# Performance work log

Measured on AMD Instinct MI355X. Metric: run time of the kernel, lower is better.

## Reference

```python
import jax, jax.numpy as jnp
import numpy as np

DECAY = 0.8

def l2norm(t):
    # F.normalize with eps=1e-12
    n = jnp.linalg.norm(t, axis=-1, keepdims=True)
    return t / jnp.maximum(n, 1e-12)

def setup_inputs() -> dict:
    key = jax.random.key(0)
    k1, k2, k3 = jax.random.split(key, 3)
    x = jax.random.normal(k1, (16, 4096, 64), dtype=jnp.float32)
    embed = l2norm(jax.random.uniform(k2, (1, 4096, 64), dtype=jnp.float32) * 2.0 - 1.0)  # uniform_init + l2norm
    cluster_size = jax.random.uniform(k3, (1, 4096), dtype=jnp.float32) * 10.0
    return {"x": x, "embed": embed, "cluster_size": cluster_size}

def reference(x, embed, cluster_size):
    # x: [b, n, d] (ndim<4 -> add codebook dim), embed: [h, c, d]
    h, c, d = embed.shape
    xh = x[None, ...]                           # [1, b, n, d]
    shape = xh.shape
    flatten = l2norm(xh.reshape(h, -1, d))      # [h, N, d]
    embed_n = l2norm(embed)                     # [h, c, d]
    dist = jnp.einsum('hnd,hcd->hnc', flatten, embed_n)          # [h, N, c]
    embed_ind_flat = jnp.argmax(dist, axis=-1)                   # temperature==0 gumbel -> argmax
    embed_onehot = jax.nn.one_hot(embed_ind_flat, c, dtype=x.dtype)  # [h, N, c]
    embed_ind = embed_ind_flat.reshape(shape[:-1])               # [h, b, n]
    # batched_embedding: gather from the raw (non-normalized) codebook
    quantize = jax.vmap(lambda e, i: e[i])(embed, embed_ind_flat).reshape(shape)  # [h, b, n, d]
    # training-mode EMA codebook update (buffer updates returned as outputs)
    bins = embed_onehot.sum(axis=1)                              # [h, c]
    new_cluster_size = cluster_size * DECAY + bins * (1.0 - DECAY)
    zero_mask = bins == 0
    bins_safe = jnp.where(zero_mask, 1.0, bins)
    embed_sum = jnp.einsum('hnd,hnc->hcd', flatten, embed_onehot)  # [h, c, d]
    embed_normalized = l2norm(embed_sum / bins_safe[..., None])
    embed_normalized = jnp.where(zero_mask[..., None], embed_n, embed_normalized)
    new_embed = embed * DECAY + embed_normalized * (1.0 - DECAY)
    # squeeze back the added codebook dim (needs_codebook_dim path)
    return quantize[0], embed_ind[0], new_embed, new_cluster_size
```

## Files before the change

kernel.cpp:

```cpp
#include <hip/hip_runtime.h>
#include <math.h>

#define DECAY 0.8f
constexpr int B_     = 16;
constexpr int NSEQ   = 4096;
constexpr int D      = 64;
constexpr int C      = 4096;
constexpr int N      = B_ * NSEQ;
constexpr int NCHUNK = 4;
constexpr int CCHUNK = C / NCHUNK;
constexpr int PANEL  = 64;
constexpr int NPANEL = CCHUNK / PANEL;

#define GATE_THR  3e-4f
#define CONS_THR  1e-3f

typedef __attribute__((ext_vector_type(8))) short bf16x8;
typedef __attribute__((ext_vector_type(4))) float f32x4;

__device__ __forceinline__ unsigned short bf16_rn(float f) {
    unsigned u = __builtin_bit_cast(unsigned, f);
    u += 0x7FFFu + ((u >> 16) & 1u);
    return (unsigned short)(u >> 16);
}
__device__ __forceinline__ float bf16_to_f(unsigned short h) {
    unsigned u = ((unsigned)h) << 16;
    return __builtin_bit_cast(float, u);
}
__device__ __forceinline__ f32x4 mfma16(bf16x8 a, bf16x8 b, f32x4 c) {
    return __builtin_amdgcn_mfma_f32_16x16x32_bf16(a, b, c, 0, 0, 0);
}

__global__ __launch_bounds__(256) void prep_e_kernel(
    const float* __restrict__ embed,
    float* __restrict__ embed_n,
    unsigned short* __restrict__ e_hi,
    unsigned short* __restrict__ e_lo,
    float* __restrict__ embed_sum,
    float* __restrict__ bins,
    int* __restrict__ dirty_count)
{
    int code = blockIdx.x * 4 + (threadIdx.x >> 6);
    int lane = threadIdx.x & 63;
    float v = embed[code * D + lane];
    float ss = v * v;
    #pragma unroll
    for (int o = 32; o > 0; o >>= 1) ss += __shfl_xor(ss, o);
    float inv = 1.0f / fmaxf(sqrtf(ss), 1e-12f);
    float en = v * inv;
    embed_n[code * D + lane] = en;

    unsigned short hi = bf16_rn(en);
    unsigned short lo = bf16_rn(en - bf16_to_f(hi));
    int g   = lane >> 3;
    int pos = code * D + ((g ^ (code & 7)) << 3) + (lane & 7);
    e_hi[pos] = hi;
    e_lo[pos] = lo;

    embed_sum[code * D + lane] = 0.0f;
    if (lane == 0) bins[code] = 0.0f;
    if (blockIdx.x == 0 && threadIdx.x == 0) *dirty_count = 0;
}

__global__ __launch_bounds__(256) void assign_mfma_kernel(
    const float* __restrict__ x,
    const unsigned short* __restrict__ e_hi,
    const unsigned short* __restrict__ e_lo,
    float* __restrict__ part)
{
    __shared__ unsigned short lds_hi[PANEL * D];
    __shared__ unsigned short lds_lo[PANEL * D];

    const int tid  = threadIdx.x;
    const int lane = tid & 63;
    const int wid  = tid >> 6;
    const int l15  = lane & 15;
    const int lg   = lane >> 4;
    const int rb   = (blockIdx.x * 4 + wid) * 32;
    const int cy   = blockIdx.y;

    bf16x8 xhi[2][2], xlo[2][2];
    #pragma unroll
    for (int g = 0; g < 2; ++g) {
        #pragma unroll
        for (int c = 0; c < 2; ++c) {
            const float* p = x + (size_t)(rb + g * 16 + l15) * D + c * 32 + lg * 8;
            float4 t0 = *(const float4*)p;
            float4 t1 = *(const float4*)(p + 4);
            float e[8] = {t0.x, t0.y, t0.z, t0.w, t1.x, t1.y, t1.z, t1.w};
            bf16x8 h, l2;
            #pragma unroll
            for (int j = 0; j < 8; ++j) {
                unsigned short hh = bf16_rn(e[j]);
                h[j]  = (short)hh;
                l2[j] = (short)bf16_rn(e[j] - bf16_to_f(hh));
            }
            xhi[g][c] = h;
            xlo[g][c] = l2;
        }
    }

    const int s7   = l15 & 7;
    const int off0 = l15 * D + (((0 + lg) ^ s7) << 3);
    const int off1 = l15 * D + (((4 + lg) ^ s7) << 3);

    float m1[2] = {-3.4e38f, -3.4e38f};
    float m2[2] = {-3.4e38f, -3.4e38f};
    int   tl[2] = {0, 0};

    for (int p = 0; p < NPANEL; ++p) {
        const int pp = cy * NPANEL + p;
        __syncthreads();
        {
            const float4* gh = (const float4*)(e_hi + (size_t)pp * PANEL * D);
            const float4* gl = (const float4*)(e_lo + (size_t)pp * PANEL * D);
            float4* lh = (float4*)lds_hi;
            float4* ll = (float4*)lds_lo;
            lh[tid]       = gh[tid];
            lh[256 + tid] = gh[256 + tid];
            ll[tid]       = gl[tid];
            ll[256 + tid] = gl[256 + tid];
        }
        __syncthreads();

        #pragma unroll
        for (int t = 0; t < PANEL / 16; ++t) {
            bf16x8 eh0 = *(const bf16x8*)(lds_hi + t * 1024 + off0);
            bf16x8 eh1 = *(const bf16x8*)(lds_hi + t * 1024 + off1);
            bf16x8 el0 = *(const bf16x8*)(lds_lo + t * 1024 + off0);
            bf16x8 el1 = *(const bf16x8*)(lds_lo + t * 1024 + off1);
            const int pt = pp * 4 + t;
            #pragma unroll
            for (int g = 0; g < 2; ++g) {
                f32x4 acc = {0.f, 0.f, 0.f, 0.f};
                acc = mfma16(eh0, xhi[g][0], acc);
                acc = mfma16(eh1, xhi[g][1], acc);
                acc = mfma16(el0, xhi[g][0], acc);
                acc = mfma16(el1, xhi[g][1], acc);
                acc = mfma16(eh0, xlo[g][0], acc);
                acc = mfma16(eh1, xlo[g][1], acc);
                float t1 = fmaxf(fmaxf(acc[0], acc[1]), fmaxf(acc[2], acc[3]));
                float mn = fminf(m1[g], t1);
                bool  gt = t1 > m1[g];
                tl[g] = gt ? pt : tl[g];
                m1[g] = fmaxf(m1[g], t1);
                m2[g] = fmaxf(m2[g], mn);
            }
        }
    }

    #pragma unroll
    for (int g = 0; g < 2; ++g) {
        float a1 = m1[g], a2 = m2[g];
        int   at = tl[g];
        #pragma unroll
        for (int d = 16; d <= 32; d <<= 1) {
            float b1 = __shfl_xor(a1, d);
            float b2 = __shfl_xor(a2, d);
            int   bt = __shfl_xor(at, d);
            float nm2 = fmaxf(fmaxf(a2, b2), fminf(a1, b1));
            bool  take = (b1 > a1);
            a1 = take ? b1 : a1;
            at = take ? bt : at;
            a2 = nm2;
        }
        if (lane < 16) {
            int row = rb + g * 16 + lane;
            float4 pr;
            pr.x = a1; pr.y = (float)at; pr.z = a2; pr.w = 0.0f;
            *reinterpret_cast<float4*>(part + (size_t)row * D + cy * 4) = pr;
        }
    }
}

__global__ __launch_bounds__(256) void merge_scatter_kernel(
    const float* __restrict__ x,
    const float* __restrict__ embed,
    const float* __restrict__ embed_n,
    float* __restrict__ q_out,
    float* __restrict__ ind_out,
    float* __restrict__ embed_sum,
    float* __restrict__ bins,
    int* __restrict__ dirty_count,
    int* __restrict__ dirty_list)
{
    int wid  = threadIdx.x >> 6;
    int lane = threadIdx.x & 63;
    int row  = blockIdx.x * 4 + wid;

    float w1a, m2x; int wt;
    {
        const float4* pp = reinterpret_cast<const float4*>(q_out + (size_t)row * D);
        float4 P = pp[0];
        w1a = P.x; wt = (int)P.y; m2x = P.z;
        #pragma unroll
        for (int j = 1; j < NCHUNK; ++j) {
            float4 Q = pp[j];
            float nm2 = fmaxf(fmaxf(m2x, Q.z), fminf(w1a, Q.x));
            if (Q.x > w1a) { w1a = Q.x; wt = (int)Q.y; }
            m2x = nm2;
        }
    }

    int   csub = lane >> 2;
    int   code = wt * 16 + csub;
    float dot;
    {
        const float4* ep = (const float4*)(embed_n + (size_t)code * D + (lane & 3) * 16);
        const float4* xp = (const float4*)(x + (size_t)row * D + (lane & 3) * 16);
        float a0 = 0.f, a1 = 0.f, a2 = 0.f, a3 = 0.f;
        #pragma unroll
        for (int k = 0; k < 4; ++k) {
            float4 e = ep[k], xx = xp[k];
            a0 = fmaf(e.x, xx.x, a0);
            a1 = fmaf(e.y, xx.y, a1);
            a2 = fmaf(e.z, xx.z, a2);
            a3 = fmaf(e.w, xx.w, a3);
        }
        dot = (a0 + a1) + (a2 + a3);
        dot += __shfl_xor(dot, 1);
        dot += __shfl_xor(dot, 2);
    }
    float v = dot, s = -3.4e38f;
    int   vi = code;
    #pragma unroll
    for (int d = 4; d <= 32; d <<= 1) {
        float bv = __shfl_xor(v, d);
        float bs = __shfl_xor(s, d);
        int   bi = __shfl_xor(vi, d);
        float ns = fmaxf(fmaxf(s, bs), fminf(v, bv));
        bool  take = (bv > v) || (bv == v && bi < vi);
        v  = take ? bv : v;
        vi = take ? bi : vi;
        s  = ns;
    }

    bool dirty = (v - m2x <= GATE_THR) || (fabsf(v - w1a) > CONS_THR);
    if (dirty) {
        if (lane == 0) {
            int slot = atomicAdd(dirty_count, 1);
            dirty_list[slot] = row;
        }
        return;
    }

    float xk = x[(size_t)row * D + lane];
    float ss = xk * xk;
    #pragma unroll
    for (int o = 32; o > 0; o >>= 1) ss += __shfl_xor(ss, o);
    float inv = 1.0f / fmaxf(sqrtf(ss), 1e-12f);

    if (lane == 0) {
        ind_out[row] = (float)vi;
        atomicAdd(&bins[vi], 1.0f);
    }
    q_out[(size_t)row * D + lane] = embed[(size_t)vi * D + lane];
    atomicAdd(&embed_sum[(size_t)vi * D + lane], xk * inv);
}

__global__ __launch_bounds__(256) void fallback_kernel(
    const float* __restrict__ x,
    const float* __restrict__ embed,
    const float* __restrict__ embed_n,
    const int* __restrict__ dirty_count,
    const int* __restrict__ dirty_list,
    float* __restrict__ ind_out,
    float* __restrict__ q_out,
    float* __restrict__ embed_sum,
    float* __restrict__ bins)
{
    __shared__ float xs[D];
    __shared__ float bv[256];
    __shared__ int   bidx[256];
    int cnt = *dirty_count;
    for (int i = blockIdx.x; i < cnt; i += gridDim.x) {
        int row = dirty_list[i];
        __syncthreads();
        if (threadIdx.x < D) xs[threadIdx.x] = x[(size_t)row * D + threadIdx.x];
        __syncthreads();
        float best = -3.4e38f;
        int   bi   = 0;
        int   c0   = threadIdx.x * 16;
        for (int c = c0; c < c0 + 16; ++c) {
            const float4* ep = (const float4*)(embed_n + (size_t)c * D);
            const float4* xp = (const float4*)xs;
            float a0 = 0.f, a1 = 0.f, a2 = 0.f, a3 = 0.f;
            #pragma unroll
            for (int k = 0; k < D / 4; ++k) {
                float4 e = ep[k], xx = xp[k];
                a0 = fmaf(e.x, xx.x, a0);
                a1 = fmaf(e.y, xx.y, a1);
                a2 = fmaf(e.z, xx.z, a2);
                a3 = fmaf(e.w, xx.w, a3);
            }
            float dd = (a0 + a1) + (a2 + a3);
            if (dd > best) { best = dd; bi = c; }
        }
        bv[threadIdx.x]   = best;
        bidx[threadIdx.x] = bi;
        __syncthreads();
        #pragma unroll
        for (int s = 128; s > 0; s >>= 1) {
            if (threadIdx.x < s) {
                float v2 = bv[threadIdx.x + s];
                int   i2 = bidx[threadIdx.x + s];
                if (v2 > bv[threadIdx.x] ||
                    (v2 == bv[threadIdx.x] && i2 < bidx[threadIdx.x])) {
                    bv[threadIdx.x]   = v2;
                    bidx[threadIdx.x] = i2;
                }
            }
            __syncthreads();
        }
        int fi = bidx[0];
        if (threadIdx.x == 0) {
            ind_out[row] = (float)fi;
            atomicAdd(&bins[fi], 1.0f);
        }
        if (threadIdx.x < 64) {
            float xk = xs[threadIdx.x];
            float ss = xk * xk;
            #pragma unroll
            for (int o = 32; o > 0; o >>= 1) ss += __shfl_xor(ss, o);
            float inv = 1.0f / fmaxf(sqrtf(ss), 1e-12f);
            q_out[(size_t)row * D + threadIdx.x] =
                embed[(size_t)fi * D + threadIdx.x];
            atomicAdd(&embed_sum[(size_t)fi * D + threadIdx.x], xk * inv);
        }
        __syncthreads();
    }
}

__global__ __launch_bounds__(256) void finalize_kernel(
    const float* __restrict__ embed,
    const float* __restrict__ cluster_size,
    const float* __restrict__ embed_n,
    const float* __restrict__ embed_sum,
    const float* __restrict__ bins,
    float* __restrict__ new_embed_out,
    float* __restrict__ new_cs_out)
{
    int code = blockIdx.x * 4 + (threadIdx.x >> 6);
    int lane = threadIdx.x & 63;
    float bsum = bins[code];
    if (lane == 0)
        new_cs_out[code] = cluster_size[code] * DECAY + bsum * (1.0f - DECAY);

    float en;
    if (bsum == 0.0f) {
        en = embed_n[code * D + lane];
    } else {
        float v = embed_sum[code * D + lane] / bsum;
        float ss = v * v;
        #pragma unroll
        for (int o = 32; o > 0; o >>= 1) ss += __shfl_xor(ss, o);
        en = v / fmaxf(sqrtf(ss), 1e-12f);
    }
    new_embed_out[code * D + lane] =
        embed[code * D + lane] * DECAY + en * (1.0f - DECAY);
}

extern "C" void kernel_launch(void* const* d_in, const int* in_sizes, int n_in,
                              void* d_out, int out_size, void* d_ws, size_t ws_size,
                              hipStream_t stream)
{
    const float* x            = (const float*)d_in[0];
    const float* embed        = (const float*)d_in[1];
    const float* cluster_size = (const float*)d_in[2];

    float* out     = (float*)d_out;
    float* q_out   = out;
    float* ind_out = out + (size_t)N * D;
    float* ne_out  = ind_out + N;
    float* ncs_out = ne_out + (size_t)C * D;

    char* ws = (char*)d_ws;
    float*          embed_n     = (float*)ws;
    float*          embed_sum   = (float*)(ws + (1u << 20));
    float*          bins        = (float*)(ws + (2u << 20));
    int*            dirty_list  = (int*)(ws + (2u << 20) + 65536);
    int*            dirty_count = (int*)(ws + (2u << 20) + 65536 + 262144);
    unsigned short* e_hi        = (unsigned short*)(ws + 3 * (1u << 20));
    unsigned short* e_lo        = (unsigned short*)(ws + 3 * (1u << 20) + 524288);

    prep_e_kernel<<<C / 4, 256, 0, stream>>>(embed, embed_n, e_hi, e_lo,
                                             embed_sum, bins, dirty_count);
    assign_mfma_kernel<<<dim3(N / 128, NCHUNK), 256, 0, stream>>>(
        x, e_hi, e_lo, q_out);
    merge_scatter_kernel<<<N / 4, 256, 0, stream>>>(x, embed, embed_n,
                                                    q_out, ind_out,
                                                    embed_sum, bins,
                                                    dirty_count, dirty_list);
    fallback_kernel<<<1024, 256, 0, stream>>>(x, embed, embed_n, dirty_count,
                                              dirty_list, ind_out, q_out,
                                              embed_sum, bins);
    finalize_kernel<<<C / 4, 256, 0, stream>>>(embed, cluster_size, embed_n,
                                               embed_sum, bins, ne_out, ncs_out);
}
```

Baseline: 173.1 us.

## Double-buffer codebook panels in LDS with direct global-to-LDS async loads

Replaces the register-staged panel copy and its two barriers with global_load_lds transfers into a double-buffered LDS panel, prefetching the next panel while the current one is consumed by MFMA. The panel size is halved to 32 codes so the two buffers fit in the same LDS footprint, and the panel tile index is rescaled to match. The goal is to hide global load latency and cut barrier stalls. In exchange there are twice as many loop iterations, each with a full vmcnt wait and barrier, and correctness depends on the swizzled layout being preserved by the linear direct copy.

```diff
diff --git a/kernel.cpp b/kernel.cpp
--- a/kernel.cpp
+++ b/kernel.cpp
@@ -9,7 +9,7 @@
 constexpr int N      = B_ * NSEQ;
 constexpr int NCHUNK = 4;
 constexpr int CCHUNK = C / NCHUNK;
-constexpr int PANEL  = 64;
+constexpr int PANEL  = 32;
 constexpr int NPANEL = CCHUNK / PANEL;
 
 #define GATE_THR  3e-4f
@@ -29,6 +29,12 @@
 }
 __device__ __forceinline__ f32x4 mfma16(bf16x8 a, bf16x8 b, f32x4 c) {
     return __builtin_amdgcn_mfma_f32_16x16x32_bf16(a, b, c, 0, 0, 0);
+}
+__device__ __forceinline__ void gload_lds16(const unsigned short* g,
+                                            unsigned short* l) {
+    __builtin_amdgcn_global_load_lds(
+        (const __attribute__((address_space(1))) unsigned int*)g,
+        (__attribute__((address_space(3))) unsigned int*)l, 16, 0, 0);
 }
 
 __global__ __launch_bounds__(256) void prep_e_kernel(
@@ -68,8 +74,8 @@
     const unsigned short* __restrict__ e_lo,
     float* __restrict__ part)
 {
-    __shared__ unsigned short lds_hi[PANEL * D];
-    __shared__ unsigned short lds_lo[PANEL * D];
+    __shared__ unsigned short lds_hi[2][PANEL * D];
+    __shared__ unsigned short lds_lo[2][PANEL * D];
 
     const int tid  = threadIdx.x;
     const int lane = tid & 63;
@@ -108,28 +114,34 @@
     float m2[2] = {-3.4e38f, -3.4e38f};
     int   tl[2] = {0, 0};
 
+    const size_t chunk_base = (size_t)cy * NPANEL * PANEL * D;
+
+    gload_lds16(e_hi + chunk_base + tid * 8, &lds_hi[0][tid * 8]);
+    gload_lds16(e_lo + chunk_base + tid * 8, &lds_lo[0][tid * 8]);
+
     for (int p = 0; p < NPANEL; ++p) {
+        const int cur = p & 1;
+        asm volatile("s_waitcnt vmcnt(0)" ::: "memory");
+        __builtin_amdgcn_s_barrier();
+        __builtin_amdgcn_sched_barrier(0);
+
+        if (p + 1 < NPANEL) {
+            const size_t nb = chunk_base + (size_t)(p + 1) * PANEL * D;
+            gload_lds16(e_hi + nb + tid * 8, &lds_hi[cur ^ 1][tid * 8]);
+            gload_lds16(e_lo + nb + tid * 8, &lds_lo[cur ^ 1][tid * 8]);
+        }
+
+        const unsigned short* Lh = lds_hi[cur];
+        const unsigned short* Ll = lds_lo[cur];
         const int pp = cy * NPANEL + p;
-        __syncthreads();
-        {
-            const float4* gh = (const float4*)(e_hi + (size_t)pp * PANEL * D);
-            const float4* gl = (const float4*)(e_lo + (size_t)pp * PANEL * D);
-            float4* lh = (float4*)lds_hi;
-            float4* ll = (float4*)lds_lo;
-            lh[tid]       = gh[tid];
-            lh[256 + tid] = gh[256 + tid];
-            ll[tid]       = gl[tid];
-            ll[256 + tid] = gl[256 + tid];
-        }
-        __syncthreads();
 
         #pragma unroll
         for (int t = 0; t < PANEL / 16; ++t) {
-            bf16x8 eh0 = *(const bf16x8*)(lds_hi + t * 1024 + off0);
-            bf16x8 eh1 = *(const bf16x8*)(lds_hi + t * 1024 + off1);
-            bf16x8 el0 = *(const bf16x8*)(lds_lo + t * 1024 + off0);
-            bf16x8 el1 = *(const bf16x8*)(lds_lo + t * 1024 + off1);
-            const int pt = pp * 4 + t;
+            bf16x8 eh0 = *(const bf16x8*)(Lh + t * 1024 + off0);
+            bf16x8 eh1 = *(const bf16x8*)(Lh + t * 1024 + off1);
+            bf16x8 el0 = *(const bf16x8*)(Ll + t * 1024 + off0);
+            bf16x8 el1 = *(const bf16x8*)(Ll + t * 1024 + off1);
+            const int pt = pp * 2 + t;
             #pragma unroll
             for (int g = 0; g < 2; ++g) {
                 f32x4 acc = {0.f, 0.f, 0.f, 0.f};
```

Result: no change. 176.1 us (+1.8%).

## Switch assignment to 32x32x16 MFMA with direct global-to-LDS tile loads

Applied to the files above, without the earlier changes.

Replaces the 16x16x32 bf16 MFMA scoring with the 32x32x16 variant, so each wave computes a 32-row by 32-code tile per step. The codebook hi/lo split is relaid into 32-code tiles that match the new operand layout, and panels are copied with global_load_lds instead of going through registers. The argmax candidate granularity becomes 32 codes per tile, and the merge kernel re-scores 32 candidates per row. This aims to raise MFMA throughput, cut LDS read instructions and shorten the staging path. The trade-offs are coarser tile gating and extra refinement work per row in the merge step.

```diff
diff --git a/kernel.cpp b/kernel.cpp
--- a/kernel.cpp
+++ b/kernel.cpp
@@ -11,12 +11,13 @@
 constexpr int CCHUNK = C / NCHUNK;
 constexpr int PANEL  = 64;
 constexpr int NPANEL = CCHUNK / PANEL;
+constexpr int TILE_ELEMS = 32 * D;
 
 #define GATE_THR  3e-4f
 #define CONS_THR  1e-3f
 
-typedef __attribute__((ext_vector_type(8))) short bf16x8;
-typedef __attribute__((ext_vector_type(4))) float f32x4;
+typedef __attribute__((ext_vector_type(8)))  short bf16x8;
+typedef __attribute__((ext_vector_type(16))) float f32x16;
 
 __device__ __forceinline__ unsigned short bf16_rn(float f) {
     unsigned u = __builtin_bit_cast(unsigned, f);
@@ -27,8 +28,14 @@
     unsigned u = ((unsigned)h) << 16;
     return __builtin_bit_cast(float, u);
 }
-__device__ __forceinline__ f32x4 mfma16(bf16x8 a, bf16x8 b, f32x4 c) {
-    return __builtin_amdgcn_mfma_f32_16x16x32_bf16(a, b, c, 0, 0, 0);
+__device__ __forceinline__ f32x16 mfma32(bf16x8 a, bf16x8 b, f32x16 c) {
+    return __builtin_amdgcn_mfma_f32_32x32x16_bf16(a, b, c, 0, 0, 0);
+}
+__device__ __forceinline__ void gload_lds16(const unsigned short* g,
+                                            unsigned short* l) {
+    __builtin_amdgcn_global_load_lds(
+        (const __attribute__((address_space(1))) unsigned int*)g,
+        (__attribute__((address_space(3))) unsigned int*)l, 16, 0, 0);
 }
 
 __global__ __launch_bounds__(256) void prep_e_kernel(
@@ -52,8 +59,9 @@
 
     unsigned short hi = bf16_rn(en);
     unsigned short lo = bf16_rn(en - bf16_to_f(hi));
-    int g   = lane >> 3;
-    int pos = code * D + ((g ^ (code & 7)) << 3) + (lane & 7);
+    int t = code >> 5, r = code & 31;
+    int g = lane >> 3, e = lane & 7;
+    size_t pos = (size_t)t * TILE_ELEMS + (g * 32 + r) * 8 + e;
     e_hi[pos] = hi;
     e_lo[pos] = lo;
 
@@ -68,108 +76,89 @@
     const unsigned short* __restrict__ e_lo,
     float* __restrict__ part)
 {
-    __shared__ unsigned short lds_hi[PANEL * D];
-    __shared__ unsigned short lds_lo[PANEL * D];
+    __shared__ unsigned short lds_hi[2 * TILE_ELEMS];
+    __shared__ unsigned short lds_lo[2 * TILE_ELEMS];
 
     const int tid  = threadIdx.x;
     const int lane = tid & 63;
     const int wid  = tid >> 6;
-    const int l15  = lane & 15;
-    const int lg   = lane >> 4;
+    const int m    = lane & 31;
+    const int hi   = lane >> 5;
     const int rb   = (blockIdx.x * 4 + wid) * 32;
     const int cy   = blockIdx.y;
 
-    bf16x8 xhi[2][2], xlo[2][2];
+    bf16x8 xhi[4], xlo[4];
     #pragma unroll
-    for (int g = 0; g < 2; ++g) {
-        #pragma unroll
-        for (int c = 0; c < 2; ++c) {
-            const float* p = x + (size_t)(rb + g * 16 + l15) * D + c * 32 + lg * 8;
-            float4 t0 = *(const float4*)p;
-            float4 t1 = *(const float4*)(p + 4);
-            float e[8] = {t0.x, t0.y, t0.z, t0.w, t1.x, t1.y, t1.z, t1.w};
-            bf16x8 h, l2;
+    for (int c = 0; c < 4; ++c) {
+        const float* p = x + (size_t)(rb + m) * D + c * 16 + hi * 8;
+        float4 t0 = *(const float4*)p;
+        float4 t1 = *(const float4*)(p + 4);
+        float e[8] = {t0.x, t0.y, t0.z, t0.w, t1.x, t1.y, t1.z, t1.w};
+        bf16x8 h, l2;
+        #pragma unroll
+        for (int j = 0; j < 8; ++j) {
+            unsigned short hh = bf16_rn(e[j]);
+            h[j]  = (short)hh;
+            l2[j] = (short)bf16_rn(e[j] - bf16_to_f(hh));
+        }
+        xhi[c] = h;
+        xlo[c] = l2;
+    }
+
+    float m1 = -3.4e38f, m2 = -3.4e38f;
+    int   tl = 0;
+
+    for (int p = 0; p < NPANEL; ++p) {
+        const size_t pbase = ((size_t)cy * NPANEL + p) * (2 * TILE_ELEMS);
+        __syncthreads();
+        gload_lds16(e_hi + pbase + tid * 8,              &lds_hi[tid * 8]);
+        gload_lds16(e_hi + pbase + TILE_ELEMS + tid * 8, &lds_hi[TILE_ELEMS + tid * 8]);
+        gload_lds16(e_lo + pbase + tid * 8,              &lds_lo[tid * 8]);
+        gload_lds16(e_lo + pbase + TILE_ELEMS + tid * 8, &lds_lo[TILE_ELEMS + tid * 8]);
+        __syncthreads();
+
+        #pragma unroll
+        for (int t = 0; t < 2; ++t) {
+            const int pt = (cy * NPANEL + p) * 2 + t;
+            f32x16 acc = {};
             #pragma unroll
-            for (int j = 0; j < 8; ++j) {
-                unsigned short hh = bf16_rn(e[j]);
-                h[j]  = (short)hh;
-                l2[j] = (short)bf16_rn(e[j] - bf16_to_f(hh));
+            for (int c = 0; c < 4; ++c) {
+                const int off = t * TILE_ELEMS + ((c * 2 + hi) * 32 + m) * 8;
+                bf16x8 eh = *(const bf16x8*)(lds_hi + off);
+                bf16x8 el = *(const bf16x8*)(lds_lo + off);
+                acc = mfma32(eh, xhi[c], acc);
+                acc = mfma32(el, xhi[c], acc);
+                acc = mfma32(eh, xlo[c], acc);
             }
-            xhi[g][c] = h;
-            xlo[g][c] = l2;
-        }
-    }
-
-    const int s7   = l15 & 7;
-    const int off0 = l15 * D + (((0 + lg) ^ s7) << 3);
-    const int off1 = l15 * D + (((4 + lg) ^ s7) << 3);
-
-    float m1[2] = {-3.4e38f, -3.4e38f};
-    float m2[2] = {-3.4e38f, -3.4e38f};
-    int   tl[2] = {0, 0};
-
-    for (int p = 0; p < NPANEL; ++p) {
-        const int pp = cy * NPANEL + p;
-        __syncthreads();
-        {
-            const float4* gh = (const float4*)(e_hi + (size_t)pp * PANEL * D);
-            const float4* gl = (const float4*)(e_lo + (size_t)pp * PANEL * D);
-            float4* lh = (float4*)lds_hi;
-            float4* ll = (float4*)lds_lo;
-            lh[tid]       = gh[tid];
-            lh[256 + tid] = gh[256 + tid];
-            ll[tid]       = gl[tid];
-            ll[256 + tid] = gl[256 + tid];
-        }
-        __syncthreads();
-
-        #pragma unroll
-        for (int t = 0; t < PANEL / 16; ++t) {
-            bf16x8 eh0 = *(const bf16x8*)(lds_hi + t * 1024 + off0);
-            bf16x8 eh1 = *(const bf16x8*)(lds_hi + t * 1024 + off1);
-            bf16x8 el0 = *(const bf16x8*)(lds_lo + t * 1024 + off0);
-            bf16x8 el1 = *(const bf16x8*)(lds_lo + t * 1024 + off1);
-            const int pt = pp * 4 + t;
-            #pragma unroll
-            for (int g = 0; g < 2; ++g) {
-                f32x4 acc = {0.f, 0.f, 0.f, 0.f};
-                acc = mfma16(eh0, xhi[g][0], acc);
-                acc = mfma16(eh1, xhi[g][1], acc);
-                acc = mfma16(el0, xhi[g][0], acc);
-                acc = mfma16(el1, xhi[g][1], acc);
-                acc = mfma16(eh0, xlo[g][0], acc);
-                acc = mfma16(eh1, xlo[g][1], acc);
-                float t1 = fmaxf(fmaxf(acc[0], acc[1]), fmaxf(acc[2], acc[3]));
-                float mn = fminf(m1[g], t1);
-                bool  gt = t1 > m1[g];
-                tl[g] = gt ? pt : tl[g];
-                m1[g] = fmaxf(m1[g], t1);
-                m2[g] = fmaxf(m2[g], mn);
-            }
-        }
-    }
-
-    #pragma unroll
-    for (int g = 0; g < 2; ++g) {
-        float a1 = m1[g], a2 = m2[g];
-        int   at = tl[g];
-        #pragma unroll
-        for (int d = 16; d <= 32; d <<= 1) {
-            float b1 = __shfl_xor(a1, d);
-            float b2 = __shfl_xor(a2, d);
-            int   bt = __shfl_xor(at, d);
-            float nm2 = fmaxf(fmaxf(a2, b2), fminf(a1, b1));
-            bool  take = (b1 > a1);
-            a1 = take ? b1 : a1;
-            at = take ? bt : at;
-            a2 = nm2;
-        }
-        if (lane < 16) {
-            int row = rb + g * 16 + lane;
-            float4 pr;
-            pr.x = a1; pr.y = (float)at; pr.z = a2; pr.w = 0.0f;
-            *reinterpret_cast<float4*>(part + (size_t)row * D + cy * 4) = pr;
-        }
+            float a = fmaxf(acc[0],  acc[1]),  b = fmaxf(acc[2],  acc[3]);
+            float c2 = fmaxf(acc[4],  acc[5]), d = fmaxf(acc[6],  acc[7]);
+            float e2 = fmaxf(acc[8],  acc[9]), f = fmaxf(acc[10], acc[11]);
+            float g2 = fmaxf(acc[12], acc[13]), h2 = fmaxf(acc[14], acc[15]);
+            float tm = fmaxf(fmaxf(fmaxf(a, b), fmaxf(c2, d)),
+                             fmaxf(fmaxf(e2, f), fmaxf(g2, h2)));
+            float mn = fminf(m1, tm);
+            bool  gt = tm > m1;
+            tl = gt ? pt : tl;
+            m1 = fmaxf(m1, tm);
+            m2 = fmaxf(m2, mn);
+        }
+    }
+
+    {
+        float b1 = __shfl_xor(m1, 32);
+        float b2 = __shfl_xor(m2, 32);
+        int   bt = __shfl_xor(tl, 32);
+        float nm2 = fmaxf(fmaxf(m2, b2), fminf(m1, b1));
+        bool  take = (b1 > m1);
+        m1 = take ? b1 : m1;
+        tl = take ? bt : tl;
+        m2 = nm2;
+    }
+    if (lane < 32) {
+        int row = rb + lane;
+        float4 pr;
+        pr.x = m1; pr.y = (float)tl; pr.z = m2; pr.w = 0.0f;
+        *reinterpret_cast<float4*>(part + (size_t)row * D + cy * 4) = pr;
     }
 }
 
@@ -202,15 +191,16 @@
         }
     }
 
-    int   csub = lane >> 2;
-    int   code = wt * 16 + csub;
+    int   c32  = lane & 31;
+    int   half = lane >> 5;
+    int   code = wt * 32 + c32;
     float dot;
     {
-        const float4* ep = (const float4*)(embed_n + (size_t)code * D + (lane & 3) * 16);
-        const float4* xp = (const float4*)(x + (size_t)row * D + (lane & 3) * 16);
+        const float4* ep = (const float4*)(embed_n + (size_t)code * D + half * 32);
+        const float4* xp = (const float4*)(x + (size_t)row * D + half * 32);
         float a0 = 0.f, a1 = 0.f, a2 = 0.f, a3 = 0.f;
         #pragma unroll
-        for (int k = 0; k < 4; ++k) {
+        for (int k = 0; k < 8; ++k) {
             float4 e = ep[k], xx = xp[k];
             a0 = fmaf(e.x, xx.x, a0);
             a1 = fmaf(e.y, xx.y, a1);
@@ -218,13 +208,12 @@
             a3 = fmaf(e.w, xx.w, a3);
         }
         dot = (a0 + a1) + (a2 + a3);
-        dot += __shfl_xor(dot, 1);
-        dot += __shfl_xor(dot, 2);
+        dot += __shfl_xor(dot, 32);
     }
     float v = dot, s = -3.4e38f;
     int   vi = code;
     #pragma unroll
-    for (int d = 4; d <= 32; d <<= 1) {
+    for (int d = 1; d <= 16; d <<= 1) {
         float bv = __shfl_xor(v, d);
         float bs = __shfl_xor(s, d);
         int   bi = __shfl_xor(vi, d);
```

After: 233.6 us. +35.0%, slower.
